# Optimization experiments

Measured on AMD Instinct MI355X. Metric: run time of the kernel, lower is better.

## Reference

```python
import jax, jax.numpy as jnp
import numpy as np


def setup_inputs() -> dict:
    key = jax.random.key(0)
    ks = jax.random.split(key, 5)
    B, C, H, W = 8, 256, 64, 64
    Cq = C // 8
    x = jax.random.normal(ks[0], (B, C, H, W), dtype=jnp.float32)
    # kaiming-uniform-ish scale for 1x1 convs (fan_in = C)
    s = float(np.sqrt(1.0 / C))
    Wq = jax.random.normal(ks[1], (Cq, C), dtype=jnp.float32) * s
    Wk = jax.random.normal(ks[2], (Cq, C), dtype=jnp.float32) * s
    Wv = jax.random.normal(ks[3], (C, C), dtype=jnp.float32) * s
    bq = jnp.zeros((Cq,), dtype=jnp.float32)
    bk = jnp.zeros((Cq,), dtype=jnp.float32)
    bv = jnp.zeros((C,), dtype=jnp.float32)
    gamma = jax.random.uniform(ks[4], (1,), dtype=jnp.float32)
    return {"x": x, "Wq": Wq, "bq": bq, "Wk": Wk, "bk": bk, "Wv": Wv, "bv": bv, "gamma": gamma}


def reference(x, Wq, bq, Wk, bk, Wv, bv, gamma):
    B, C, H, W = x.shape
    flat = x.reshape(B, C, H * W)                       # [B, C, N]
    # 1x1 conv == channel matmul
    q = jnp.einsum('oc,bcn->bon', Wq, flat) + bq[None, :, None]   # [B, C/8, N]
    k = jnp.einsum('oc,bcn->bon', Wk, flat) + bk[None, :, None]   # [B, C/8, N]
    v = jnp.einsum('oc,bcn->bon', Wv, flat) + bv[None, :, None]   # [B, C,   N]
    # query permuted to [B, N, C/8]; query_key = bmm -> [B, N, N]
    qk = jnp.einsum('bcn,bcm->bnm', q, k)               # [B, N, N]
    attn = jax.nn.softmax(qk, axis=1)                   # softmax over dim=1 (non-standard)
    out = jnp.einsum('bcn,bnm->bcm', v, attn)           # [B, C, N]
    out = out.reshape(B, C, H, W)
    return gamma[0] * out + x
```

## Files before the change

### kernel.cpp

```cpp
#include <hip/hip_runtime.h>
#include <hip/hip_bf16.h>

#define B_   8
#define C_   256
#define CQ_  32
#define N_   4096
#define OC_  320

typedef __bf16 bf16;
typedef __attribute__((ext_vector_type(8))) __bf16 bf16x8;
typedef __attribute__((ext_vector_type(4))) __bf16 bf16x4;
typedef __attribute__((ext_vector_type(4))) float f32x4;

#define LOG2E 1.4426950408889634f

#define QT_OFF ((size_t)0)
#define KT_OFF ((size_t)B_*N_*CQ_)
#define VB_OFF ((size_t)2*B_*N_*CQ_)
#define WB_OFF (VB_OFF + (size_t)B_*C_*N_)
#define XT_OFF (WB_OFF + (size_t)OC_*C_)
#define WS_END_BF16 (XT_OFF + (size_t)B_*N_*C_)
#define BIAS_BYTE (WS_END_BF16*2)
#define WS_BYTES (BIAS_BYTE + OC_*4)

__device__ inline float exp2_hw(float x) {
  return __builtin_amdgcn_exp2f(x);
}

__global__ __launch_bounds__(256) void prep_w(
    const float* __restrict__ Wq, const float* __restrict__ bq,
    const float* __restrict__ Wk, const float* __restrict__ bk,
    const float* __restrict__ Wv, const float* __restrict__ bv,
    bf16* __restrict__ ws)
{
  const int idx = blockIdx.x*256 + threadIdx.x;
  const int o = idx >> 8, c = idx & 255;
  const float v = (o < 32) ? Wq[o*C_ + c]
                : (o < 64) ? Wk[(o-32)*C_ + c]
                           : Wv[(o-64)*C_ + c];
  ws[WB_OFF + idx] = (bf16)v;
  if (idx < OC_) {
    const float bb = (idx < 32) ? bq[idx] : (idx < 64) ? bk[idx-32] : bv[idx-64];
    ((float*)((char*)ws + BIAS_BYTE))[idx] = bb;
  }
}

__global__ __launch_bounds__(256) void prep_x(
    const float* __restrict__ x, bf16* __restrict__ ws)
{
  const int b  = blockIdx.z;
  const int n  = blockIdx.x*64 + (threadIdx.x & 63);
  const int c0 = blockIdx.y*32 + (threadIdx.x >> 6)*8;
  const float* xp = x + ((size_t)b*C_ + c0)*N_ + n;
  bf16x8 pk;
  #pragma unroll
  for (int j = 0; j < 8; ++j) pk[j] = (bf16)xp[(size_t)j*N_];
  *(bf16x8*)(ws + XT_OFF + ((size_t)b*N_ + n)*C_ + c0) = pk;
}

__global__ __launch_bounds__(256) void qkv_mfma(
    const bf16* __restrict__ wsc, bf16* __restrict__ ws)
{
  const int b   = blockIdx.y;
  const int n0  = blockIdx.x * 64;
  const int tid = threadIdx.x, lane = tid & 63;
  const int w   = __builtin_amdgcn_readfirstlane(tid >> 6);
  const int lm  = lane & 15, g = lane >> 4;
  const int obase = w*80;

  const bf16*  Wb   = wsc + WB_OFF;
  const bf16*  xT   = wsc + XT_OFF + (size_t)b*N_*C_;
  const float* bias = (const float*)((const char*)wsc + BIAS_BYTE);

  f32x4 acc[5][4];
  #pragma unroll
  for (int ot = 0; ot < 5; ++ot)
    #pragma unroll
    for (int nt = 0; nt < 4; ++nt)
      acc[ot][nt] = (f32x4){0.f, 0.f, 0.f, 0.f};

  for (int kk = 0; kk < 8; ++kk) {
    bf16x8 wa[5], xf[4];
    #pragma unroll
    for (int ot = 0; ot < 5; ++ot)
      wa[ot] = *(const bf16x8*)(Wb + (size_t)(obase + ot*16 + lm)*C_ + kk*32 + g*8);
    #pragma unroll
    for (int nt = 0; nt < 4; ++nt)
      xf[nt] = *(const bf16x8*)(xT + (size_t)(n0 + nt*16 + lm)*C_ + kk*32 + g*8);
    #pragma unroll
    for (int ot = 0; ot < 5; ++ot)
      #pragma unroll
      for (int nt = 0; nt < 4; ++nt)
        acc[ot][nt] = __builtin_amdgcn_mfma_f32_16x16x32_bf16(
                        wa[ot], xf[nt], acc[ot][nt], 0, 0, 0);
  }

  float bv4[5][4];
  #pragma unroll
  for (int ot = 0; ot < 5; ++ot)
    #pragma unroll
    for (int r = 0; r < 4; ++r)
      bv4[ot][r] = bias[obase + ot*16 + g*4 + r];

  bf16* qT = ws + QT_OFF + (size_t)b*N_*CQ_;
  bf16* kT = ws + KT_OFF + (size_t)b*N_*CQ_;
  bf16* vb = ws + VB_OFF + (size_t)b*C_*N_;

  #pragma unroll
  for (int ot = 0; ot < 5; ++ot) {
    const int O = obase + ot*16;
    #pragma unroll
    for (int nt = 0; nt < 4; ++nt) {
      const int n = n0 + nt*16 + lm;
      if (O < 32) {
        bf16x4 pk;
        #pragma unroll
        for (int r = 0; r < 4; ++r)
          pk[r] = (bf16)((acc[ot][nt][r] + bv4[ot][r]) * LOG2E);
        *(bf16x4*)(qT + (size_t)n*CQ_ + O + g*4) = pk;
      } else if (O < 64) {
        bf16x4 pk;
        #pragma unroll
        for (int r = 0; r < 4; ++r) pk[r] = (bf16)(acc[ot][nt][r] + bv4[ot][r]);
        *(bf16x4*)(kT + (size_t)n*CQ_ + (O - 32) + g*4) = pk;
      } else {
        #pragma unroll
        for (int r = 0; r < 4; ++r)
          vb[(size_t)(O - 64 + g*4 + r)*N_ + n] = (bf16)(acc[ot][nt][r] + bv4[ot][r]);
      }
    }
  }
}

__global__ __launch_bounds__(256) void attn_kernel(
    const bf16* __restrict__ ws, const float* __restrict__ x,
    const float* __restrict__ gamma, float* __restrict__ out)
{
  const int bid  = blockIdx.x;
  const int b    = bid & 7;
  const int m0   = (bid >> 3) << 6;
  const int tid  = threadIdx.x;
  const int lane = tid & 63;
  const int w    = __builtin_amdgcn_readfirstlane(tid >> 6);
  const int lm   = lane & 15;
  const int g    = lane >> 4;

  const bf16* qT = ws + QT_OFF + (size_t)b*N_*CQ_;
  const bf16* kT = ws + KT_OFF + (size_t)b*N_*CQ_;
  const bf16* vb = ws + VB_OFF + (size_t)b*C_*N_;

  __shared__ __align__(16) char Pb[2][64*128];
  __shared__ float red[4][64];
  __shared__ float dsh[64];

  bf16x8 kb[4];
  #pragma unroll
  for (int ms = 0; ms < 4; ++ms)
    kb[ms] = *(const bf16x8*)(kT + (size_t)(m0 + ms*16 + lm)*CQ_ + g*8);

  f32x4 acc[4][4];
  #pragma unroll
  for (int cs = 0; cs < 4; ++cs)
    #pragma unroll
    for (int ms = 0; ms < 4; ++ms)
      acc[cs][ms] = (f32x4){0.f, 0.f, 0.f, 0.f};
  float colsum[4] = {0.f, 0.f, 0.f, 0.f};

  const int c0  = w*64;
  const int swb = w*32 + g*8;
  const f32x4 zero4 = (f32x4){0.f, 0.f, 0.f, 0.f};

  for (int t = 0; t < 64; ++t) {
    const int n0 = t*64;

    bf16x8 vf[4][2];
    #pragma unroll
    for (int cs = 0; cs < 4; ++cs)
      #pragma unroll
      for (int kc = 0; kc < 2; ++kc)
        vf[cs][kc] = *(const bf16x8*)(vb + (size_t)(c0 + cs*16 + lm)*N_
                                         + n0 + kc*32 + g*8);

    bf16x8 qf = *(const bf16x8*)(qT + (size_t)(n0 + w*16 + lm)*CQ_ + g*8);
    f32x4 s[4];
    #pragma unroll
    for (int ms = 0; ms < 4; ++ms)
      s[ms] = __builtin_amdgcn_mfma_f32_16x16x32_bf16(qf, kb[ms], zero4, 0, 0, 0);

    char* pbuf = Pb[t & 1];
    #pragma unroll
    for (int ms = 0; ms < 4; ++ms) {
      float p0 = exp2_hw(s[ms][0]);
      float p1 = exp2_hw(s[ms][1]);
      float p2 = exp2_hw(s[ms][2]);
      float p3 = exp2_hw(s[ms][3]);
      colsum[ms] += (p0 + p1) + (p2 + p3);
      bf16x4 pk;
      pk[0] = (bf16)p0; pk[1] = (bf16)p1; pk[2] = (bf16)p2; pk[3] = (bf16)p3;
      const int m = lm + 16*ms;
      *(bf16x4*)(pbuf + m*128 + (swb ^ ((m & 7) << 4))) = pk;
    }
    __syncthreads();

    #pragma unroll
    for (int kc = 0; kc < 2; ++kc)
      #pragma unroll
      for (int ms = 0; ms < 4; ++ms) {
        const int m = lm + 16*ms;
        bf16x8 pf = *(const bf16x8*)(pbuf + m*128
                                     + ((kc*64 + g*16) ^ ((m & 7) << 4)));
        #pragma unroll
        for (int cs = 0; cs < 4; ++cs)
          acc[cs][ms] = __builtin_amdgcn_mfma_f32_16x16x32_bf16(
                          vf[cs][kc], pf, acc[cs][ms], 0, 0, 0);
      }
  }

  #pragma unroll
  for (int ms = 0; ms < 4; ++ms) {
    colsum[ms] += __shfl_xor(colsum[ms], 16, 64);
    colsum[ms] += __shfl_xor(colsum[ms], 32, 64);
  }
  if (lane < 16) {
    #pragma unroll
    for (int ms = 0; ms < 4; ++ms) red[w][lm + 16*ms] = colsum[ms];
  }
  __syncthreads();
  if (tid < 64) dsh[tid] = red[0][tid] + red[1][tid] + red[2][tid] + red[3][tid];
  __syncthreads();

  const float gam = gamma[0];
  float inv[4];
  #pragma unroll
  for (int ms = 0; ms < 4; ++ms) inv[ms] = gam / dsh[lm + 16*ms];

  #pragma unroll
  for (int cs = 0; cs < 4; ++cs)
    #pragma unroll
    for (int ms = 0; ms < 4; ++ms)
      #pragma unroll
      for (int r = 0; r < 4; ++r) {
        const int c = c0 + cs*16 + g*4 + r;
        const int m = m0 + 16*ms + lm;
        const size_t idx = ((size_t)b*C_ + c)*N_ + m;
        out[idx] = acc[cs][ms][r] * inv[ms] + x[idx];
      }
}

extern "C" void kernel_launch(void* const* d_in, const int* in_sizes, int n_in,
                              void* d_out, int out_size, void* d_ws, size_t ws_size,
                              hipStream_t stream) {
  const float* x     = (const float*)d_in[0];
  const float* Wq    = (const float*)d_in[1];
  const float* bq    = (const float*)d_in[2];
  const float* Wk    = (const float*)d_in[3];
  const float* bk    = (const float*)d_in[4];
  const float* Wv    = (const float*)d_in[5];
  const float* bv    = (const float*)d_in[6];
  const float* gamma = (const float*)d_in[7];
  float* out = (float*)d_out;
  bf16* ws   = (bf16*)d_ws;

  if (ws_size < WS_BYTES) return;

  prep_w<<<320, 256, 0, stream>>>(Wq, bq, Wk, bk, Wv, bv, ws);
  prep_x<<<dim3(64, 8, 8), 256, 0, stream>>>(x, ws);
  qkv_mfma<<<dim3(64, 8), 256, 0, stream>>>(ws, ws);
  attn_kernel<<<512, 256, 0, stream>>>(ws, x, gamma, out);
}
```

Measured before the change: 174.4 us.

## Keep attention probabilities in registers, drop LDS exchange and barriers

The attention kernel now has each wave compute the full QK^T tile for its own 32-row chunk of n. It picks the Q row mapping so that the MFMA output layout of exp2(S) directly forms the B-operand fragment of the P·V MFMA. This removes the shared-memory P buffer, the per-iteration __syncthreads, and the cross-wave column-sum reduction. In exchange every wave recomputes all QK^T scores, which is 4x redundant score MFMAs and exp2 work. Launch bounds now request 2 blocks per SIMD to raise occupancy.

```diff
diff --git a/kernel.cpp b/kernel.cpp
--- a/kernel.cpp
+++ b/kernel.cpp
@@ -132,7 +132,7 @@
   }
 }
 
-__global__ __launch_bounds__(256) void attn_kernel(
+__global__ __launch_bounds__(256, 2) void attn_kernel(
     const bf16* __restrict__ ws, const float* __restrict__ x,
     const float* __restrict__ gamma, float* __restrict__ out)
 {
@@ -149,10 +149,6 @@
   const bf16* kT = ws + KT_OFF + (size_t)b*N_*CQ_;
   const bf16* vb = ws + VB_OFF + (size_t)b*C_*N_;
 
-  __shared__ __align__(16) char Pb[2][64*128];
-  __shared__ float red[4][64];
-  __shared__ float dsh[64];
-
   bf16x8 kb[4];
   #pragma unroll
   for (int ms = 0; ms < 4; ++ms)
@@ -166,54 +162,53 @@
       acc[cs][ms] = (f32x4){0.f, 0.f, 0.f, 0.f};
   float colsum[4] = {0.f, 0.f, 0.f, 0.f};
 
-  const int c0  = w*64;
-  const int swb = w*32 + g*8;
+  const int c0 = w*64;
   const f32x4 zero4 = (f32x4){0.f, 0.f, 0.f, 0.f};
 
-  for (int t = 0; t < 64; ++t) {
-    const int n0 = t*64;
-
-    bf16x8 vf[4][2];
+  const bf16* qpb = qT + (size_t)(8*(lm >> 2) + (lm & 3))*CQ_ + g*8;
+  const bf16* vpb = vb + (size_t)(c0 + lm)*N_ + g*8;
+
+  for (int t = 0; t < 128; ++t) {
+    const size_t n0 = (size_t)t * 32;
+
+    bf16x8 qf0 = *(const bf16x8*)(qpb + n0*CQ_);
+    bf16x8 qf1 = *(const bf16x8*)(qpb + n0*CQ_ + 4*CQ_);
+    bf16x8 vf[4];
+    #pragma unroll
+    for (int cs = 0; cs < 4; ++cs)
+      vf[cs] = *(const bf16x8*)(vpb + (size_t)cs*16*N_ + n0);
+
+    f32x4 s0[4], s1[4];
+    #pragma unroll
+    for (int ms = 0; ms < 4; ++ms) {
+      s0[ms] = __builtin_amdgcn_mfma_f32_16x16x32_bf16(qf0, kb[ms], zero4, 0, 0, 0);
+      s1[ms] = __builtin_amdgcn_mfma_f32_16x16x32_bf16(qf1, kb[ms], zero4, 0, 0, 0);
+    }
+
+    bf16x8 pfrag[4];
+    #pragma unroll
+    for (int ms = 0; ms < 4; ++ms) {
+      float e0 = exp2_hw(s0[ms][0]);
+      float e1 = exp2_hw(s0[ms][1]);
+      float e2 = exp2_hw(s0[ms][2]);
+      float e3 = exp2_hw(s0[ms][3]);
+      float e4 = exp2_hw(s1[ms][0]);
+      float e5 = exp2_hw(s1[ms][1]);
+      float e6 = exp2_hw(s1[ms][2]);
+      float e7 = exp2_hw(s1[ms][3]);
+      colsum[ms] += ((e0 + e1) + (e2 + e3)) + ((e4 + e5) + (e6 + e7));
+      bf16x8 pf;
+      pf[0] = (bf16)e0; pf[1] = (bf16)e1; pf[2] = (bf16)e2; pf[3] = (bf16)e3;
+      pf[4] = (bf16)e4; pf[5] = (bf16)e5; pf[6] = (bf16)e6; pf[7] = (bf16)e7;
+      pfrag[ms] = pf;
+    }
+
     #pragma unroll
     for (int cs = 0; cs < 4; ++cs)
       #pragma unroll
-      for (int kc = 0; kc < 2; ++kc)
-        vf[cs][kc] = *(const bf16x8*)(vb + (size_t)(c0 + cs*16 + lm)*N_
-                                         + n0 + kc*32 + g*8);
-
-    bf16x8 qf = *(const bf16x8*)(qT + (size_t)(n0 + w*16 + lm)*CQ_ + g*8);
-    f32x4 s[4];
-    #pragma unroll
-    for (int ms = 0; ms < 4; ++ms)
-      s[ms] = __builtin_amdgcn_mfma_f32_16x16x32_bf16(qf, kb[ms], zero4, 0, 0, 0);
-
-    char* pbuf = Pb[t & 1];
-    #pragma unroll
-    for (int ms = 0; ms < 4; ++ms) {
-      float p0 = exp2_hw(s[ms][0]);
-      float p1 = exp2_hw(s[ms][1]);
-      float p2 = exp2_hw(s[ms][2]);
-      float p3 = exp2_hw(s[ms][3]);
-      colsum[ms] += (p0 + p1) + (p2 + p3);
-      bf16x4 pk;
-      pk[0] = (bf16)p0; pk[1] = (bf16)p1; pk[2] = (bf16)p2; pk[3] = (bf16)p3;
-      const int m = lm + 16*ms;
-      *(bf16x4*)(pbuf + m*128 + (swb ^ ((m & 7) << 4))) = pk;
-    }
-    __syncthreads();
-
-    #pragma unroll
-    for (int kc = 0; kc < 2; ++kc)
-      #pragma unroll
-      for (int ms = 0; ms < 4; ++ms) {
-        const int m = lm + 16*ms;
-        bf16x8 pf = *(const bf16x8*)(pbuf + m*128
-                                     + ((kc*64 + g*16) ^ ((m & 7) << 4)));
-        #pragma unroll
-        for (int cs = 0; cs < 4; ++cs)
-          acc[cs][ms] = __builtin_amdgcn_mfma_f32_16x16x32_bf16(
-                          vf[cs][kc], pf, acc[cs][ms], 0, 0, 0);
-      }
+      for (int ms = 0; ms < 4; ++ms)
+        acc[cs][ms] = __builtin_amdgcn_mfma_f32_16x16x32_bf16(
+                        vf[cs], pfrag[ms], acc[cs][ms], 0, 0, 0);
   }
 
   #pragma unroll
@@ -221,18 +216,11 @@
     colsum[ms] += __shfl_xor(colsum[ms], 16, 64);
     colsum[ms] += __shfl_xor(colsum[ms], 32, 64);
   }
-  if (lane < 16) {
-    #pragma unroll
-    for (int ms = 0; ms < 4; ++ms) red[w][lm + 16*ms] = colsum[ms];
-  }
-  __syncthreads();
-  if (tid < 64) dsh[tid] = red[0][tid] + red[1][tid] + red[2][tid] + red[3][tid];
-  __syncthreads();
 
   const float gam = gamma[0];
   float inv[4];
   #pragma unroll
-  for (int ms = 0; ms < 4; ++ms) inv[ms] = gam / dsh[lm + 16*ms];
+  for (int ms = 0; ms < 4; ++ms) inv[ms] = gam / colsum[ms];
 
   #pragma unroll
   for (int cs = 0; cs < 4; ++cs)
```

Result: slower. 193.3 us (+10.9%).
